# Performance work log

Measured on AMD Instinct MI355X. Metric: run time of the kernel, lower is better.

Reference implementation:

```python
import jax, jax.numpy as jnp
import numpy as np

N = 131072       # active sparse sites (fixed)
C_IN = 256       # FPN input channels
HID = 512        # CONV_HEAD_DIM
K = 9            # 3x3 kernel taps
LAYERS = 8       # NUM_STACKED_CONVS
GROUPS = 32      # GroupNorm groups (detectron2 default)
EPS = 1e-5


def _build_rulebook(rng):
    # Sample sparse occupancy over 64 ROIs of 64x64, build 3x3 neighbor map.
    B, H, W = 64, 64, 64
    mask = rng.random((B, H, W)) < 0.60
    coords = np.argwhere(mask)[:N]          # [N,3] (b,y,x), fixed N
    assert coords.shape[0] == N
    grid = -np.ones((B, H + 2, W + 2), np.int32)  # padded, -1 = inactive
    grid[coords[:, 0], coords[:, 1] + 1, coords[:, 2] + 1] = np.arange(N, dtype=np.int32)
    offs = [(dy, dx) for dy in (-1, 0, 1) for dx in (-1, 0, 1)]
    nbr = np.stack(
        [grid[coords[:, 0], coords[:, 1] + 1 + dy, coords[:, 2] + 1 + dx] for dy, dx in offs],
        axis=1,
    )  # [N,9], -1 where neighbor inactive (submanifold: output sites == input sites)
    return nbr


def setup_inputs() -> dict:
    rng = np.random.default_rng(0)
    nbr = _build_rulebook(rng)
    key = jax.random.key(0)
    k0, k1, k2, k3, k4 = jax.random.split(key, 5)
    features = jax.random.normal(k0, (N, C_IN), jnp.float32)
    w0 = jax.random.normal(k1, (K, C_IN, HID), jnp.float32) * (1.0 / np.sqrt(K * C_IN))
    w_rest = jax.random.normal(k2, (LAYERS - 1, K, HID, HID), jnp.float32) * (1.0 / np.sqrt(K * HID))
    gamma = 1.0 + 0.1 * jax.random.normal(k3, (LAYERS, HID), jnp.float32)
    beta = 0.1 * jax.random.normal(k4, (LAYERS, HID), jnp.float32)
    return {
        "features": features,
        "nbr_idx": jnp.asarray(nbr),
        "w0": w0,
        "w_rest": w_rest,
        "gamma": gamma,
        "beta": beta,
    }


def _subm_conv(x, nbr_idx, w):
    # gather-GEMM-scatter submanifold conv: x [N,Cin], nbr_idx [N,K], w [K,Cin,Cout]
    n = x.shape[0]
    xp = jnp.concatenate([x, jnp.zeros((1, x.shape[1]), x.dtype)], axis=0)  # zero row for -1
    idx = jnp.where(nbr_idx < 0, n, nbr_idx)
    out = jnp.zeros((n, w.shape[2]), x.dtype)
    for k in range(K):  # fixed small loop over kernel taps
        out = out + xp[idx[:, k]] @ w[k]
    return out


def _group_norm(x, g, b):
    # per-point GroupNorm over channel groups: x [N,C]
    n, c = x.shape
    xg = x.reshape(n, GROUPS, c // GROUPS)
    mu = jnp.mean(xg, axis=-1, keepdims=True)
    var = jnp.var(xg, axis=-1, keepdims=True)
    xg = (xg - mu) * jax.lax.rsqrt(var + EPS)
    return xg.reshape(n, c) * g + b


def reference(features, nbr_idx, w0, w_rest, gamma, beta):
    x = jax.nn.relu(_group_norm(_subm_conv(features, nbr_idx, w0), gamma[0], beta[0]))
    for i in range(LAYERS - 1):
        x = jax.nn.relu(_group_norm(_subm_conv(x, nbr_idx, w_rest[i]), gamma[i + 1], beta[i + 1]))
    return x
```

## Files before the change

kernel.cpp:

```cpp
#include <hip/hip_runtime.h>
#include <stdint.h>

#define N_SITES 131072
#define CIN0 256
#define HID 512
#define KTAPS 9
#define NLAYERS 8

typedef __bf16 bf16x8 __attribute__((ext_vector_type(8)));
typedef float f32x4 __attribute__((ext_vector_type(4)));

__device__ __forceinline__ unsigned short f2bf(float f) {
    union { float f; unsigned u; } v; v.f = f;
    return (unsigned short)((v.u + 0x7fffu + ((v.u >> 16) & 1u)) >> 16);
}


__global__ void cvt_features_kernel(const float* __restrict__ in, unsigned short* __restrict__ out) {
    int t = blockIdx.x * 256 + threadIdx.x;
    const float4* p = (const float4*)in + 2 * (size_t)t;
    float4 a = p[0], b = p[1];
    uint4 o;
    o.x = f2bf(a.x) | ((unsigned)f2bf(a.y) << 16);
    o.y = f2bf(a.z) | ((unsigned)f2bf(a.w) << 16);
    o.z = f2bf(b.x) | ((unsigned)f2bf(b.y) << 16);
    o.w = f2bf(b.z) | ((unsigned)f2bf(b.w) << 16);
    ((uint4*)out)[t] = o;
}

__global__ void zero_rows_kernel(unsigned short* __restrict__ x) {
    int t = threadIdx.x;
    x[(size_t)N_SITES * 256 + t] = 0;
    x[(size_t)N_SITES * 512 + t] = 0;
    x[(size_t)N_SITES * 512 + 256 + t] = 0;
}

__global__ void transpose_w_kernel(const float* __restrict__ in, unsigned short* __restrict__ out, int cin) {
    __shared__ float tile[32][33];
    int m = blockIdx.z;
    int nb = blockIdx.x * 32;
    int cb = blockIdx.y * 32;
    int tx = threadIdx.x, ty = threadIdx.y;
    const float* src = in + (size_t)m * cin * HID;
    unsigned short* dst = out + (size_t)m * HID * cin;
#pragma unroll
    for (int j = 0; j < 4; ++j) {
        int r = ty + 8 * j;
        tile[r][tx] = src[(size_t)(cb + r) * HID + nb + tx];
    }
    __syncthreads();
#pragma unroll
    for (int j = 0; j < 4; ++j) {
        int r = ty + 8 * j;
        dst[(size_t)(nb + r) * cin + cb + tx] = f2bf(tile[tx][r]);
    }
}


__device__ __forceinline__ void async16(const void* g, void* l) {
    __builtin_amdgcn_global_load_lds(
        (__attribute__((address_space(1))) unsigned int*)(g),
        (__attribute__((address_space(3))) unsigned int*)(l),
        16, 0, 0);
}

__global__ __launch_bounds__(256, 4) void subm_gemm_kernel(
    const unsigned short* __restrict__ x,
    const int* __restrict__ nbr,
    const unsigned short* __restrict__ wt,
    float* __restrict__ out,
    int cin)
{
    __shared__ uint4 As[1024];
    __shared__ uint4 Bs[1024];

    const int tid = threadIdx.x;
    const int lane = tid & 63;
    const int wave = tid >> 6;

    const int b = (int)blockIdx.x;
    const int xcd = b & 7;
    const int slot = b >> 3;
    const int colbase = (xcd & 3) * 128;
    const int rowbase = ((xcd >> 2) * 512 + slot) * 128;

    const int wm = (wave >> 1) * 64;
    const int wn = (wave & 1) * 64;

    const int r0 = tid >> 3;
    const int cs = tid & 7;
    const int chunk = cs ^ (r0 & 7);
    const int ldsbase = tid & ~63;
    const int kiters = cin >> 6;

    const f32x4 zero4 = {0.f, 0.f, 0.f, 0.f};
    f32x4 acc[4][4];
#pragma unroll
    for (int i = 0; i < 4; ++i)
#pragma unroll
        for (int j = 0; j < 4; ++j)
            acc[i][j] = zero4;

    for (int tap = 0; tap < KTAPS; ++tap) {
        const unsigned short* arow[4];
#pragma unroll
        for (int i = 0; i < 4; ++i) {
            int idx = nbr[(size_t)(rowbase + r0 + 32 * i) * KTAPS + tap];
            if (idx < 0) idx = N_SITES;
            arow[i] = x + (size_t)idx * cin + chunk * 8;
        }
        const unsigned short* wbase = wt + ((size_t)tap * HID + colbase) * cin + chunk * 8;
        const unsigned short* brow[4];
#pragma unroll
        for (int i = 0; i < 4; ++i)
            brow[i] = wbase + (size_t)(r0 + 32 * i) * cin;

        for (int kk = 0; kk < kiters; ++kk) {
            const int ko = kk * 64;
            __syncthreads();
#pragma unroll
            for (int i = 0; i < 4; ++i) {
                async16(arow[i] + ko, &As[ldsbase + 256 * i]);
                async16(brow[i] + ko, &Bs[ldsbase + 256 * i]);
            }
            __syncthreads();

#pragma unroll
            for (int ks = 0; ks < 2; ++ks) {
                bf16x8 af[4], bfr[4];
#pragma unroll
                for (int f = 0; f < 4; ++f) {
                    int rl = wm + f * 16 + (lane & 15);
                    int ch = ks * 4 + (lane >> 4);
                    af[f]  = __builtin_bit_cast(bf16x8, As[rl * 8 + (ch ^ (rl & 7))]);
                    int cl = wn + f * 16 + (lane & 15);
                    bfr[f] = __builtin_bit_cast(bf16x8, Bs[cl * 8 + (ch ^ (cl & 7))]);
                }
#pragma unroll
                for (int i = 0; i < 4; ++i)
#pragma unroll
                    for (int j = 0; j < 4; ++j)
                        acc[i][j] = __builtin_amdgcn_mfma_f32_16x16x32_bf16(af[i], bfr[j], acc[i][j], 0, 0, 0);
            }
        }
    }

#pragma unroll
    for (int i = 0; i < 4; ++i) {
        int grow = rowbase + wm + i * 16 + (lane >> 4) * 4;
#pragma unroll
        for (int j = 0; j < 4; ++j) {
            int gcol = colbase + wn + j * 16 + (lane & 15);
#pragma unroll
            for (int r = 0; r < 4; ++r)
                out[(size_t)(grow + r) * HID + gcol] = acc[i][j][r];
        }
    }
}


__global__ void gn_relu_kernel(const float* __restrict__ conv,
                               const float* __restrict__ gamma,
                               const float* __restrict__ beta,
                               unsigned short* __restrict__ bf_out,
                               float* __restrict__ f_out,
                               int write_bf16)
{
    int row = blockIdx.x * 4 + (threadIdx.x >> 6);
    int lane = threadIdx.x & 63;
    const float4* src = (const float4*)(conv + (size_t)row * HID);
    float4 a = src[lane];
    float4 b = src[64 + lane];
    float sa = a.x + a.y + a.z + a.w;
    float qa = a.x * a.x + a.y * a.y + a.z * a.z + a.w * a.w;
    float sb = b.x + b.y + b.z + b.w;
    float qb = b.x * b.x + b.y * b.y + b.z * b.z + b.w * b.w;
    sa += __shfl_xor(sa, 1); qa += __shfl_xor(qa, 1);
    sa += __shfl_xor(sa, 2); qa += __shfl_xor(qa, 2);
    sb += __shfl_xor(sb, 1); qb += __shfl_xor(qb, 1);
    sb += __shfl_xor(sb, 2); qb += __shfl_xor(qb, 2);
    float ma = sa * 0.0625f;
    float ra = rsqrtf(qa * 0.0625f - ma * ma + 1e-5f);
    float mb = sb * 0.0625f;
    float rb = rsqrtf(qb * 0.0625f - mb * mb + 1e-5f);

    const float4* g4 = (const float4*)gamma;
    const float4* b4 = (const float4*)beta;
    float4 ga = g4[lane], gb = g4[64 + lane];
    float4 ba = b4[lane], bb = b4[64 + lane];
    float4 ya, yb;
    ya.x = fmaxf(0.f, (a.x - ma) * ra * ga.x + ba.x);
    ya.y = fmaxf(0.f, (a.y - ma) * ra * ga.y + ba.y);
    ya.z = fmaxf(0.f, (a.z - ma) * ra * ga.z + ba.z);
    ya.w = fmaxf(0.f, (a.w - ma) * ra * ga.w + ba.w);
    yb.x = fmaxf(0.f, (b.x - mb) * rb * gb.x + bb.x);
    yb.y = fmaxf(0.f, (b.y - mb) * rb * gb.y + bb.y);
    yb.z = fmaxf(0.f, (b.z - mb) * rb * gb.z + bb.z);
    yb.w = fmaxf(0.f, (b.w - mb) * rb * gb.w + bb.w);

    if (write_bf16) {
        uint2* dst = (uint2*)(bf_out + (size_t)row * HID);
        uint2 pa, pb;
        pa.x = f2bf(ya.x) | ((unsigned)f2bf(ya.y) << 16);
        pa.y = f2bf(ya.z) | ((unsigned)f2bf(ya.w) << 16);
        pb.x = f2bf(yb.x) | ((unsigned)f2bf(yb.y) << 16);
        pb.y = f2bf(yb.z) | ((unsigned)f2bf(yb.w) << 16);
        dst[lane] = pa;
        dst[64 + lane] = pb;
    } else {
        float4* dst = (float4*)(f_out + (size_t)row * HID);
        dst[lane] = ya;
        dst[64 + lane] = yb;
    }
}


extern "C" void kernel_launch(void* const* d_in, const int* in_sizes, int n_in,
                              void* d_out, int out_size, void* d_ws, size_t ws_size,
                              hipStream_t stream) {
    const float* features = (const float*)d_in[0];
    const int*   nbr      = (const int*)d_in[1];
    const float* w0       = (const float*)d_in[2];
    const float* w_rest   = (const float*)d_in[3];
    const float* gamma    = (const float*)d_in[4];
    const float* beta     = (const float*)d_in[5];
    float* out = (float*)d_out;

    unsigned short* xbuf = (unsigned short*)d_ws;
    size_t xbytes = (size_t)(N_SITES + 1) * HID * sizeof(unsigned short);
    unsigned short* w0t = (unsigned short*)((char*)d_ws + xbytes);
    size_t w0t_bytes = (size_t)KTAPS * HID * CIN0 * sizeof(unsigned short);
    unsigned short* wrt = (unsigned short*)((char*)d_ws + xbytes + w0t_bytes);

    cvt_features_kernel<<<N_SITES * CIN0 / (256 * 8), 256, 0, stream>>>(features, xbuf);
    zero_rows_kernel<<<1, 256, 0, stream>>>(xbuf);
    transpose_w_kernel<<<dim3(HID / 32, CIN0 / 32, KTAPS), dim3(32, 8), 0, stream>>>(w0, w0t, CIN0);
    transpose_w_kernel<<<dim3(HID / 32, HID / 32, (NLAYERS - 1) * KTAPS), dim3(32, 8), 0, stream>>>(w_rest, wrt, HID);

    for (int l = 0; l < NLAYERS; ++l) {
        const unsigned short* wt = (l == 0) ? w0t : wrt + (size_t)(l - 1) * KTAPS * HID * HID;
        int cin = (l == 0) ? CIN0 : HID;
        subm_gemm_kernel<<<(N_SITES / 128) * 4, 256, 0, stream>>>(xbuf, nbr, wt, out, cin);
        gn_relu_kernel<<<N_SITES / 4, 256, 0, stream>>>(out, gamma + (size_t)l * HID, beta + (size_t)l * HID,
                                                        xbuf, out, (l < NLAYERS - 1) ? 1 : 0);
    }
}
```

Before: 5.355 ms.

## Fuse GroupNorm and ReLU into the sparse conv GEMM epilogue

Removes the separate GroupNorm+ReLU kernel. Each 16-column MFMA tile already covers exactly one GN group, so the group statistics are reduced with lane shuffles in registers and the normalized bf16 (or final fp32) result is written straight out. Activations now ping-pong between the workspace and the output buffer, which is reused as bf16 scratch. This drops the fp32 intermediate write and re-read per layer. In exchange the epilogue issues narrow scattered 2-byte stores and adds register pressure.

New measurement: 5.314 ms. No clear change (-0.8%).

```diff
diff --git a/kernel.cpp b/kernel.cpp
--- a/kernel.cpp
+++ b/kernel.cpp
@@ -28,11 +28,13 @@
     ((uint4*)out)[t] = o;
 }
 
-__global__ void zero_rows_kernel(unsigned short* __restrict__ x) {
+__global__ void zero_rows_kernel(unsigned short* __restrict__ xf, unsigned short* __restrict__ xo) {
     int t = threadIdx.x;
-    x[(size_t)N_SITES * 256 + t] = 0;
-    x[(size_t)N_SITES * 512 + t] = 0;
-    x[(size_t)N_SITES * 512 + 256 + t] = 0;
+    xf[(size_t)N_SITES * 512 + t] = 0;
+    xf[(size_t)N_SITES * 512 + 256 + t] = 0;
+    xo[(size_t)N_SITES * 256 + t] = 0;
+    xo[(size_t)N_SITES * 512 + t] = 0;
+    xo[(size_t)N_SITES * 512 + 256 + t] = 0;
 }
 
 __global__ void transpose_w_kernel(const float* __restrict__ in, unsigned short* __restrict__ out, int cin) {
@@ -64,12 +66,14 @@
         16, 0, 0);
 }
 
-__global__ __launch_bounds__(256, 4) void subm_gemm_kernel(
+__global__ __launch_bounds__(256, 4) void subm_gemm_gn_kernel(
     const unsigned short* __restrict__ x,
     const int* __restrict__ nbr,
     const unsigned short* __restrict__ wt,
-    float* __restrict__ out,
-    int cin)
+    const float* __restrict__ gamma,
+    const float* __restrict__ beta,
+    void* __restrict__ obuf,
+    int cin, int write_bf16)
 {
     __shared__ uint4 As[1024];
     __shared__ uint4 Bs[1024];
@@ -145,72 +149,51 @@
         }
     }
 
+    float gv[4], bv[4];
+#pragma unroll
+    for (int j = 0; j < 4; ++j) {
+        int gcol = colbase + wn + j * 16 + (lane & 15);
+        gv[j] = gamma[gcol];
+        bv[j] = beta[gcol];
+    }
+
+    unsigned short* bf_out = (unsigned short*)obuf;
+    float* f_out = (float*)obuf;
+
 #pragma unroll
     for (int i = 0; i < 4; ++i) {
-        int grow = rowbase + wm + i * 16 + (lane >> 4) * 4;
+        const int grow = rowbase + wm + i * 16 + (lane >> 4) * 4;
 #pragma unroll
         for (int j = 0; j < 4; ++j) {
-            int gcol = colbase + wn + j * 16 + (lane & 15);
-#pragma unroll
-            for (int r = 0; r < 4; ++r)
-                out[(size_t)(grow + r) * HID + gcol] = acc[i][j][r];
+            const int gcol = colbase + wn + j * 16 + (lane & 15);
+            f32x4 v = acc[i][j];
+            f32x4 s = v;
+            f32x4 q = v * v;
+#pragma unroll
+            for (int m = 1; m < 16; m <<= 1) {
+#pragma unroll
+                for (int r = 0; r < 4; ++r) {
+                    s[r] += __shfl_xor(s[r], m);
+                    q[r] += __shfl_xor(q[r], m);
+                }
+            }
+            f32x4 y;
+#pragma unroll
+            for (int r = 0; r < 4; ++r) {
+                float mu = s[r] * 0.0625f;
+                float rstd = rsqrtf(q[r] * 0.0625f - mu * mu + 1e-5f);
+                y[r] = fmaxf(0.f, (v[r] - mu) * rstd * gv[j] + bv[j]);
+            }
+            if (write_bf16) {
+#pragma unroll
+                for (int r = 0; r < 4; ++r)
+                    bf_out[(size_t)(grow + r) * HID + gcol] = f2bf(y[r]);
+            } else {
+#pragma unroll
+                for (int r = 0; r < 4; ++r)
+                    f_out[(size_t)(grow + r) * HID + gcol] = y[r];
+            }
         }
-    }
-}
-
-
-__global__ void gn_relu_kernel(const float* __restrict__ conv,
-                               const float* __restrict__ gamma,
-                               const float* __restrict__ beta,
-                               unsigned short* __restrict__ bf_out,
-                               float* __restrict__ f_out,
-                               int write_bf16)
-{
-    int row = blockIdx.x * 4 + (threadIdx.x >> 6);
-    int lane = threadIdx.x & 63;
-    const float4* src = (const float4*)(conv + (size_t)row * HID);
-    float4 a = src[lane];
-    float4 b = src[64 + lane];
-    float sa = a.x + a.y + a.z + a.w;
-    float qa = a.x * a.x + a.y * a.y + a.z * a.z + a.w * a.w;
-    float sb = b.x + b.y + b.z + b.w;
-    float qb = b.x * b.x + b.y * b.y + b.z * b.z + b.w * b.w;
-    sa += __shfl_xor(sa, 1); qa += __shfl_xor(qa, 1);
-    sa += __shfl_xor(sa, 2); qa += __shfl_xor(qa, 2);
-    sb += __shfl_xor(sb, 1); qb += __shfl_xor(qb, 1);
-    sb += __shfl_xor(sb, 2); qb += __shfl_xor(qb, 2);
-    float ma = sa * 0.0625f;
-    float ra = rsqrtf(qa * 0.0625f - ma * ma + 1e-5f);
-    float mb = sb * 0.0625f;
-    float rb = rsqrtf(qb * 0.0625f - mb * mb + 1e-5f);
-
-    const float4* g4 = (const float4*)gamma;
-    const float4* b4 = (const float4*)beta;
-    float4 ga = g4[lane], gb = g4[64 + lane];
-    float4 ba = b4[lane], bb = b4[64 + lane];
-    float4 ya, yb;
-    ya.x = fmaxf(0.f, (a.x - ma) * ra * ga.x + ba.x);
-    ya.y = fmaxf(0.f, (a.y - ma) * ra * ga.y + ba.y);
-    ya.z = fmaxf(0.f, (a.z - ma) * ra * ga.z + ba.z);
-    ya.w = fmaxf(0.f, (a.w - ma) * ra * ga.w + ba.w);
-    yb.x = fmaxf(0.f, (b.x - mb) * rb * gb.x + bb.x);
-    yb.y = fmaxf(0.f, (b.y - mb) * rb * gb.y + bb.y);
-    yb.z = fmaxf(0.f, (b.z - mb) * rb * gb.z + bb.z);
-    yb.w = fmaxf(0.f, (b.w - mb) * rb * gb.w + bb.w);
-
-    if (write_bf16) {
-        uint2* dst = (uint2*)(bf_out + (size_t)row * HID);
-        uint2 pa, pb;
-        pa.x = f2bf(ya.x) | ((unsigned)f2bf(ya.y) << 16);
-        pa.y = f2bf(ya.z) | ((unsigned)f2bf(ya.w) << 16);
-        pb.x = f2bf(yb.x) | ((unsigned)f2bf(yb.y) << 16);
-        pb.y = f2bf(yb.z) | ((unsigned)f2bf(yb.w) << 16);
-        dst[lane] = pa;
-        dst[64 + lane] = pb;
-    } else {
-        float4* dst = (float4*)(f_out + (size_t)row * HID);
-        dst[lane] = ya;
-        dst[64 + lane] = yb;
     }
 }
 
@@ -224,24 +207,26 @@
     const float* w_rest   = (const float*)d_in[3];
     const float* gamma    = (const float*)d_in[4];
     const float* beta     = (const float*)d_in[5];
-    float* out = (float*)d_out;
-
-    unsigned short* xbuf = (unsigned short*)d_ws;
+
+    unsigned short* xF = (unsigned short*)d_ws;
     size_t xbytes = (size_t)(N_SITES + 1) * HID * sizeof(unsigned short);
     unsigned short* w0t = (unsigned short*)((char*)d_ws + xbytes);
     size_t w0t_bytes = (size_t)KTAPS * HID * CIN0 * sizeof(unsigned short);
     unsigned short* wrt = (unsigned short*)((char*)d_ws + xbytes + w0t_bytes);
-
-    cvt_features_kernel<<<N_SITES * CIN0 / (256 * 8), 256, 0, stream>>>(features, xbuf);
-    zero_rows_kernel<<<1, 256, 0, stream>>>(xbuf);
+    unsigned short* xO = (unsigned short*)d_out;
+
+    cvt_features_kernel<<<N_SITES * CIN0 / (256 * 8), 256, 0, stream>>>(features, xO);
+    zero_rows_kernel<<<1, 256, 0, stream>>>(xF, xO);
     transpose_w_kernel<<<dim3(HID / 32, CIN0 / 32, KTAPS), dim3(32, 8), 0, stream>>>(w0, w0t, CIN0);
     transpose_w_kernel<<<dim3(HID / 32, HID / 32, (NLAYERS - 1) * KTAPS), dim3(32, 8), 0, stream>>>(w_rest, wrt, HID);
 
     for (int l = 0; l < NLAYERS; ++l) {
         const unsigned short* wt = (l == 0) ? w0t : wrt + (size_t)(l - 1) * KTAPS * HID * HID;
         int cin = (l == 0) ? CIN0 : HID;
-        subm_gemm_kernel<<<(N_SITES / 128) * 4, 256, 0, stream>>>(xbuf, nbr, wt, out, cin);
-        gn_relu_kernel<<<N_SITES / 4, 256, 0, stream>>>(out, gamma + (size_t)l * HID, beta + (size_t)l * HID,
-                                                        xbuf, out, (l < NLAYERS - 1) ? 1 : 0);
-    }
-}
+        const unsigned short* xin = (l & 1) ? xF : xO;
+        void* obuf = (l == NLAYERS - 1) ? d_out : (void*)((l & 1) ? xO : xF);
+        subm_gemm_gn_kernel<<<(N_SITES / 128) * 4, 256, 0, stream>>>(
+            xin, nbr, wt, gamma + (size_t)l * HID, beta + (size_t)l * HID,
+            obuf, cin, (l < NLAYERS - 1) ? 1 : 0);
+    }
+}
```
